# Kernel optimization log

Measured on AMD Instinct MI355X. Metric: run time of the kernel, lower is better.

Reference implementation:

```python
import jax, jax.numpy as jnp
import numpy as np

B, N, D_IN, D_OUT = 8, 2048, 256, 128
ROW_ZERO = 85 - 10  # hardcoded in original: a[:, 0:85-10] = 0 (zeros rows, dim 1)
NEG_BIG = -9.0e15
EPS = 1e-12  # F.normalize eps


def setup_inputs() -> dict:
    key = jax.random.key(0)
    k1, k2, k3, k4 = jax.random.split(key, 4)
    h = jax.random.normal(k1, (B, N, D_IN), dtype=jnp.float32)
    adj = jax.random.randint(k2, (B, N, N), 0, 2, dtype=jnp.int32)
    adj_eye = jax.random.randint(k3, (B, N, N), 0, 2, dtype=jnp.int32)
    # xavier_uniform with gain=1.414 for W [in, out]
    limit = 1.414 * np.sqrt(6.0 / (D_IN + D_OUT))
    W = jax.random.uniform(k4, (D_IN, D_OUT), minval=-limit, maxval=limit, dtype=jnp.float32)
    return {"h": h, "adj": adj, "adj_eye": adj_eye, "W": W}


def reference(h, adj, adj_eye, W):
    # Wh: [B, N, D_OUT]
    Wh = jnp.matmul(h, W)
    # L2-normalize along feature dim (F.normalize semantics: x / max(||x||, eps))
    norm = jnp.maximum(jnp.linalg.norm(Wh, axis=-1, keepdims=True), EPS)
    Whn = Wh / norm
    # dense cosine-similarity scores: [B, N, N]
    score = jnp.einsum("bnd,bmd->bnm", Whn, Whn)
    # double-sort top-k emulation (faithful to original, incl. row-wise zeroing bug)
    a_sorted = jnp.sort(score, axis=-1)
    idx1 = jnp.argsort(score, axis=-1)
    a_sorted = a_sorted.at[:, 0:ROW_ZERO, :].set(0.0)
    idx2 = jnp.argsort(idx1, axis=-1)  # inverse permutation
    attscore = jnp.take_along_axis(a_sorted, idx2, axis=-1)
    # adjacency mask + softmax over neighbors
    e = jnp.where(adj_eye > 0, attscore, NEG_BIG)
    attention = jax.nn.softmax(e, axis=-1)
    # (dropout is identity in eval mode)
    h_prime = jnp.matmul(attention, Wh)
    return jax.nn.elu(h_prime)
```

## Files before the change

### kernel.cpp

```cpp
#include <hip/hip_runtime.h>
#include <stdint.h>

#define NN   2048
#define DD   128
#define DIN  256
#define ROWZ 75

typedef float f32x4 __attribute__((ext_vector_type(4)));
typedef short bf16x8 __attribute__((ext_vector_type(8)));
typedef unsigned int u32x2 __attribute__((ext_vector_type(2)));

__device__ __forceinline__ unsigned short f2bf(float x){
  union { float f; unsigned int u; } v; v.f = x;
  unsigned int u = v.u;
  u += 0x7fffu + ((u >> 16) & 1u);
  return (unsigned short)(u >> 16);
}
__device__ __forceinline__ float bf2f(unsigned short b){
  union { float f; unsigned int u; } v; v.u = ((unsigned int)b) << 16;
  return v.f;
}

__launch_bounds__(512, 2)
__global__ void wh_kernel(const float* __restrict__ h, const float* __restrict__ W,
                          unsigned short* __restrict__ whn, unsigned short* __restrict__ whT)
{
  __shared__ unsigned short WhiT[128][40];
  __shared__ unsigned short WloT[128][40];
  __shared__ float ssp[64][3];
  __shared__ float sinv_s[64];

  const int t    = threadIdx.x;
  const int bid  = blockIdx.x;
  const int r0   = ((bid & 7) << 11) | ((bid >> 3) << 6);
  const int w    = t >> 6;
  const int l    = t & 63;
  const int quad = l >> 4;
  const int l16  = l & 15;
  const int wr   = (w & 3) * 16;
  const int nc   = (w >> 2) * 64;
  const int ch   = w >> 2;

  const int sd = t & 127;
  const int sk = (t >> 7) * 8;

  f32x4 acc[4], occ[4];
#pragma unroll
  for (int ns = 0; ns < 4; ++ns){
    acc[ns] = (f32x4){0.f,0.f,0.f,0.f};
    occ[ns] = (f32x4){0.f,0.f,0.f,0.f};
  }

  float wv[8];
#pragma unroll
  for (int j = 0; j < 8; ++j) wv[j] = W[(size_t)(sk + j) * DD + sd];
  const float* hrow = h + (size_t)(r0 + wr + l16) * DIN;
  f32x4 hv0 = *(const f32x4*)(hrow + quad*8);
  f32x4 hv1 = *(const f32x4*)(hrow + quad*8 + 4);

  for (int kt = 0; kt < 8; ++kt){
    __syncthreads();
    {
      bf16x8 whi8, wlo8;
#pragma unroll
      for (int j = 0; j < 8; ++j){
        float x = wv[j];
        unsigned short hb = f2bf(x);
        whi8[j] = (short)hb;
        wlo8[j] = (short)f2bf(x - bf2f(hb));
      }
      *(bf16x8*)&WhiT[sd][sk] = whi8;
      *(bf16x8*)&WloT[sd][sk] = wlo8;
    }
    bf16x8 ahi, alo;
#pragma unroll
    for (int e = 0; e < 4; ++e){
      unsigned short hb0 = f2bf(hv0[e]), hb1 = f2bf(hv1[e]);
      ahi[e]   = (short)hb0;  alo[e]   = (short)f2bf(hv0[e] - bf2f(hb0));
      ahi[4+e] = (short)hb1;  alo[4+e] = (short)f2bf(hv1[e] - bf2f(hb1));
    }
    __syncthreads();

    if (kt < 7){
      const int k0n = (kt + 1) * 32;
#pragma unroll
      for (int j = 0; j < 8; ++j) wv[j] = W[(size_t)(k0n + sk + j) * DD + sd];
      hv0 = *(const f32x4*)(hrow + k0n + quad*8);
      hv1 = *(const f32x4*)(hrow + k0n + quad*8 + 4);
    }

#pragma unroll
    for (int ns = 0; ns < 4; ++ns){
      bf16x8 bhi = *(const bf16x8*)&WhiT[nc + ns*16 + l16][quad*8];
      bf16x8 blo = *(const bf16x8*)&WloT[nc + ns*16 + l16][quad*8];
      acc[ns] = __builtin_amdgcn_mfma_f32_16x16x32_bf16(ahi, bhi, acc[ns], 0, 0, 0);
      acc[ns] = __builtin_amdgcn_mfma_f32_16x16x32_bf16(alo, bhi, acc[ns], 0, 0, 0);
      acc[ns] = __builtin_amdgcn_mfma_f32_16x16x32_bf16(ahi, blo, acc[ns], 0, 0, 0);
      occ[ns] = __builtin_amdgcn_mfma_f32_16x16x32_bf16(bhi, ahi, occ[ns], 0, 0, 0);
      occ[ns] = __builtin_amdgcn_mfma_f32_16x16x32_bf16(bhi, alo, occ[ns], 0, 0, 0);
      occ[ns] = __builtin_amdgcn_mfma_f32_16x16x32_bf16(blo, ahi, occ[ns], 0, 0, 0);
    }
  }

#pragma unroll
  for (int r = 0; r < 4; ++r){
    float val = 0.f;
#pragma unroll
    for (int ns = 0; ns < 4; ++ns) val += acc[ns][r] * acc[ns][r];
    val += __shfl_xor(val, 1);
    val += __shfl_xor(val, 2);
    val += __shfl_xor(val, 4);
    val += __shfl_xor(val, 8);
    if (l16 == 0) ssp[wr + quad*4 + r][ch] = val;
  }
  __syncthreads();
  if (t < 64){
    float ss = ssp[t][0] + ssp[t][1];
    sinv_s[t] = 1.0f / fmaxf(sqrtf(ss), 1e-12f);
  }
  __syncthreads();

  const int bb = r0 >> 11;
  const int n0 = (r0 & 2047) + wr;

#pragma unroll
  for (int ns = 0; ns < 4; ++ns)
#pragma unroll
    for (int r = 0; r < 4; ++r){
      const int row = wr + quad*4 + r;
      whn[(size_t)(r0 + row) * DD + nc + ns*16 + l16] = f2bf(acc[ns][r] * sinv_s[row]);
    }
#pragma unroll
  for (int ns = 0; ns < 4; ++ns)
#pragma unroll
    for (int r = 0; r < 4; ++r){
      const int d = nc + ns*16 + quad*4 + r;
      whT[((size_t)(bb * DD + d)) * NN + n0 + l16] = f2bf(occ[ns][r]);
    }
}

__launch_bounds__(512, 2)
__global__ void attn_kernel(const unsigned short* __restrict__ whn,
                            const unsigned short* __restrict__ whT,
                            const int* __restrict__ adje,
                            float* __restrict__ out)
{
  __shared__ unsigned short Kt[2][128 * 128];
  __shared__ unsigned short Vt[2][128 * 128];
  __shared__ unsigned short Pbuf[8][32 * 40];
  __shared__ float linv_s[64];

  const int t    = threadIdx.x;
  const int w    = t >> 6;
  const int l    = t & 63;
  const int quad = l >> 4;
  const int l16  = l & 15;
  const int qh   = w >> 2;
  const int ms   = w & 3;
  const int b     = blockIdx.x & 7;
  const int qbase = (blockIdx.x >> 3) * 64;

  const unsigned short* whn_b = whn + (size_t)b * NN * DD;
  const unsigned short* whT_b = whT + (size_t)b * DD * NN;
  const int*            adj_b = adje + (size_t)b * NN * NN;

#define STAGE(M0, CC)                                                          \
  if (w < 4){                                                                  \
    _Pragma("unroll")                                                          \
    for (int ii = 0; ii < 8; ++ii){                                            \
      const int row = w*32 + ii*4 + (l >> 4);                                  \
      const unsigned short* src = whn_b + (size_t)((M0) + row) * DD            \
                                  + (l16 ^ (row & 7)) * 8;                     \
      __builtin_amdgcn_global_load_lds(                                        \
          (const __attribute__((address_space(1))) void*)src,                  \
          (__attribute__((address_space(3))) void*)&Kt[CC][(w*32 + ii*4)*128], \
          16, 0, 0);                                                           \
    }                                                                          \
  } else {                                                                     \
    _Pragma("unroll")                                                          \
    for (int ii = 0; ii < 8; ++ii){                                            \
      const int dv = (w-4)*32 + ii*4 + (l >> 4);                               \
      const unsigned short* src = whT_b + (size_t)dv * NN + (M0)               \
                                  + (l16 ^ (dv & 7)) * 8;                      \
      __builtin_amdgcn_global_load_lds(                                        \
          (const __attribute__((address_space(1))) void*)src,                  \
          (__attribute__((address_space(3))) void*)&Vt[CC][((w-4)*32+ii*4)*128],\
          16, 0, 0);                                                           \
    }                                                                          \
  }

  bf16x8 qf[2][4];
#pragma unroll
  for (int s = 0; s < 2; ++s)
#pragma unroll
    for (int kc = 0; kc < 4; ++kc)
      qf[s][kc] = *(const bf16x8*)(whn_b + (size_t)(qbase + qh*32 + s*16 + l16) * DD + kc*32 + quad*8);

  f32x4 oacc[2][8];
  float lacc[2][4];
#pragma unroll
  for (int s = 0; s < 2; ++s){
#pragma unroll
    for (int dt = 0; dt < 8; ++dt) oacc[s][dt] = (f32x4){0.f, 0.f, 0.f, 0.f};
#pragma unroll
    for (int r = 0; r < 4; ++r) lacc[s][r] = 0.f;
  }

  unsigned short* const Pw = &Pbuf[w][0];

  int av[2][2][4];
#pragma unroll
  for (int f = 0; f < 2; ++f)
#pragma unroll
    for (int s = 0; s < 2; ++s)
#pragma unroll
      for (int r = 0; r < 4; ++r)
        av[f][s][r] = adj_b[(size_t)(qbase + qh*32 + s*16 + quad*4 + r) * NN + ms*32 + f*16 + l16];
  STAGE(0, 0)
  __syncthreads();

  for (int it = 0; it < 16; ++it){
    const int m0  = it * 128;
    const int cur = it & 1;

    int avn[2][2][4];
    if (it < 15){
      const int mn = m0 + 128;
#pragma unroll
      for (int f = 0; f < 2; ++f)
#pragma unroll
        for (int s = 0; s < 2; ++s)
#pragma unroll
          for (int r = 0; r < 4; ++r)
            avn[f][s][r] = adj_b[(size_t)(qbase + qh*32 + s*16 + quad*4 + r) * NN + mn + ms*32 + f*16 + l16];
      STAGE(mn, cur ^ 1)
    }

    bf16x8 kf[2][4];
#pragma unroll
    for (int f = 0; f < 2; ++f)
#pragma unroll
      for (int kc = 0; kc < 4; ++kc){
        const int row = ms*32 + f*16 + l16;
        kf[f][kc] = *(const bf16x8*)&Kt[cur][row*128 + (((kc*4 + quad) ^ (l16 & 7)) * 8)];
      }
#pragma unroll
    for (int f = 0; f < 2; ++f){
#pragma unroll
      for (int s = 0; s < 2; ++s){
        f32x4 sc = (f32x4){0.f, 0.f, 0.f, 0.f};
#pragma unroll
        for (int kc = 0; kc < 4; ++kc)
          sc = __builtin_amdgcn_mfma_f32_16x16x32_bf16(qf[s][kc], kf[f][kc], sc, 0, 0, 0);
#pragma unroll
        for (int r = 0; r < 4; ++r){
          const int qrow = qbase + qh*32 + s*16 + quad*4 + r;
          float sv = (qrow < ROWZ) ? 0.f : sc[r];
          float p32 = (av[f][s][r] > 0) ? __expf(sv) : 0.f;
          unsigned short pb = f2bf(p32);
          lacc[s][r] += bf2f(pb);
          Pw[(s*16 + quad*4 + r) * 40 + f*16 + l16] = pb;
        }
      }
    }

    bf16x8 pfr0 = *(const bf16x8*)&Pw[(l16) * 40 + quad*8];
    bf16x8 pfr1 = *(const bf16x8*)&Pw[(16 + l16) * 40 + quad*8];
    __builtin_amdgcn_s_setprio(1);
#pragma unroll
    for (int dt = 0; dt < 8; ++dt){
      const int d = dt*16 + l16;
      bf16x8 vf = *(const bf16x8*)&Vt[cur][d*128 + (((ms*4 + quad) ^ (l16 & 7)) * 8)];
      oacc[0][dt] = __builtin_amdgcn_mfma_f32_16x16x32_bf16(pfr0, vf, oacc[0][dt], 0, 0, 0);
      oacc[1][dt] = __builtin_amdgcn_mfma_f32_16x16x32_bf16(pfr1, vf, oacc[1][dt], 0, 0, 0);
    }
    __builtin_amdgcn_s_setprio(0);

    __builtin_amdgcn_sched_barrier(0);
    asm volatile("s_waitcnt vmcnt(0)" ::: "memory");
    __builtin_amdgcn_sched_barrier(0);
    __builtin_amdgcn_s_barrier();
    __builtin_amdgcn_sched_barrier(0);

    if (it < 15){
#pragma unroll
      for (int f = 0; f < 2; ++f)
#pragma unroll
        for (int s = 0; s < 2; ++s)
#pragma unroll
          for (int r = 0; r < 4; ++r)
            av[f][s][r] = avn[f][s][r];
    }
  }

  {
    float* fl = (float*)&Pbuf[0][0];
#pragma unroll
    for (int s = 0; s < 2; ++s)
#pragma unroll
      for (int r = 0; r < 4; ++r)
        fl[(qh*32 + s*16 + quad*4 + r) * 64 + ms*16 + l16] = lacc[s][r];
  }
  __syncthreads();
  if (t < 64){
    const float* fl = (const float*)&Pbuf[0][0];
    float sum = 0.f;
#pragma unroll
    for (int c = 0; c < 64; ++c) sum += fl[t * 64 + c];
    linv_s[t] = 1.0f / sum;
  }

  float* const owf = (float*)&Kt[0][0];
  for (int s = 0; s < 2; ++s){
    __syncthreads();
#pragma unroll
    for (int dt = 0; dt < 8; ++dt)
#pragma unroll
      for (int r = 0; r < 4; ++r)
        owf[w*2048 + (quad*4 + r)*128 + dt*16 + l16] = oacc[s][dt][r];
    __syncthreads();
#pragma unroll
    for (int j = 0; j < 8; ++j){
      const int o     = j*512 + t;
      const int row32 = o >> 7;
      const int d     = o & 127;
      const int qh2   = row32 >> 4;
      const int r16   = row32 & 15;
      float v = owf[(qh2*4 + 0)*2048 + r16*128 + d]
              + owf[(qh2*4 + 1)*2048 + r16*128 + d]
              + owf[(qh2*4 + 2)*2048 + r16*128 + d]
              + owf[(qh2*4 + 3)*2048 + r16*128 + d];
      const int qrl = qh2*32 + s*16 + r16;
      v *= linv_s[qrl];
      v = (v > 0.f) ? v : expm1f(v);
      out[(size_t)(b*NN + qbase + qrl) * DD + d] = v;
    }
  }
#undef STAGE
}

extern "C" void kernel_launch(void* const* d_in, const int* in_sizes, int n_in,
                              void* d_out, int out_size, void* d_ws, size_t ws_size,
                              hipStream_t stream)
{
  const float* h       = (const float*)d_in[0];
  const int*   adj_eye = (const int*)d_in[2];
  const float* W       = (const float*)d_in[3];
  float*       out     = (float*)d_out;

  unsigned short* whn  = (unsigned short*)d_ws;
  unsigned short* whT  = whn + (size_t)16384 * 128;

  wh_kernel<<<256, 512, 0, stream>>>(h, W, whn, whT);
  attn_kernel<<<256, 512, 0, stream>>>(whn, whT, adj_eye, out);
}
```

Before: 282.7 us.

## Pack adjacency mask into bitmasks in the Wh kernel before attention

Adds 256 extra blocks to the first kernel that read the int32 adjacency matrix and compress it into 64-bit ballot bitmasks in workspace. The attention kernel then reads 32-bit mask words per row instead of int32 values per element, which cuts the bytes it loads from global memory. The full int32 adjacency matrix still has to be read once by the packing blocks, adding a write and read of the small packed mask and extra work in the first launch. The attention mask loads are now issued in the same iteration they are used rather than prefetched one step ahead, which may expose their latency.

```diff
diff --git a/kernel.cpp b/kernel.cpp
--- a/kernel.cpp
+++ b/kernel.cpp
@@ -22,16 +22,45 @@
 }
 
 __launch_bounds__(512, 2)
-__global__ void wh_kernel(const float* __restrict__ h, const float* __restrict__ W,
-                          unsigned short* __restrict__ whn, unsigned short* __restrict__ whT)
+__global__ void wh_pack_kernel(const float* __restrict__ h, const float* __restrict__ W,
+                               const int* __restrict__ adje,
+                               unsigned short* __restrict__ whn, unsigned short* __restrict__ whT,
+                               unsigned long long* __restrict__ adjp)
 {
+  const int t   = threadIdx.x;
+  const int bid = blockIdx.x;
+
+  if (bid >= 256){
+    const int pb = bid - 256;
+    const int wv = t >> 6;
+    const int ln = t & 63;
+#pragma unroll 1
+    for (int rr = 0; rr < 8; ++rr){
+      const int grow = pb * 64 + wv * 8 + rr;
+      const int* arow = adje + (size_t)grow * NN;
+      unsigned long long* drow = adjp + (size_t)grow * 32;
+#pragma unroll 1
+      for (int cb = 0; cb < 2; ++cb){
+        int pv[16];
+#pragma unroll
+        for (int j = 0; j < 16; ++j) pv[j] = arow[(cb*16 + j) * 64 + ln];
+        unsigned long long m[16];
+#pragma unroll
+        for (int j = 0; j < 16; ++j) m[j] = __ballot(pv[j] > 0);
+        if (ln == 0){
+#pragma unroll
+          for (int j = 0; j < 16; ++j) drow[cb*16 + j] = m[j];
+        }
+      }
+    }
+    return;
+  }
+
   __shared__ unsigned short WhiT[128][40];
   __shared__ unsigned short WloT[128][40];
   __shared__ float ssp[64][3];
   __shared__ float sinv_s[64];
 
-  const int t    = threadIdx.x;
-  const int bid  = blockIdx.x;
   const int r0   = ((bid & 7) << 11) | ((bid >> 3) << 6);
   const int w    = t >> 6;
   const int l    = t & 63;
@@ -51,9 +80,9 @@
     occ[ns] = (f32x4){0.f,0.f,0.f,0.f};
   }
 
-  float wv[8];
-#pragma unroll
-  for (int j = 0; j < 8; ++j) wv[j] = W[(size_t)(sk + j) * DD + sd];
+  float wv8[8];
+#pragma unroll
+  for (int j = 0; j < 8; ++j) wv8[j] = W[(size_t)(sk + j) * DD + sd];
   const float* hrow = h + (size_t)(r0 + wr + l16) * DIN;
   f32x4 hv0 = *(const f32x4*)(hrow + quad*8);
   f32x4 hv1 = *(const f32x4*)(hrow + quad*8 + 4);
@@ -64,7 +93,7 @@
       bf16x8 whi8, wlo8;
 #pragma unroll
       for (int j = 0; j < 8; ++j){
-        float x = wv[j];
+        float x = wv8[j];
         unsigned short hb = f2bf(x);
         whi8[j] = (short)hb;
         wlo8[j] = (short)f2bf(x - bf2f(hb));
@@ -84,7 +113,7 @@
     if (kt < 7){
       const int k0n = (kt + 1) * 32;
 #pragma unroll
-      for (int j = 0; j < 8; ++j) wv[j] = W[(size_t)(k0n + sk + j) * DD + sd];
+      for (int j = 0; j < 8; ++j) wv8[j] = W[(size_t)(k0n + sk + j) * DD + sd];
       hv0 = *(const f32x4*)(hrow + k0n + quad*8);
       hv1 = *(const f32x4*)(hrow + k0n + quad*8 + 4);
     }
@@ -142,7 +171,7 @@
 __launch_bounds__(512, 2)
 __global__ void attn_kernel(const unsigned short* __restrict__ whn,
                             const unsigned short* __restrict__ whT,
-                            const int* __restrict__ adje,
+                            const unsigned int* __restrict__ adjp,
                             float* __restrict__ out)
 {
   __shared__ unsigned short Kt[2][128 * 128];
@@ -162,7 +191,7 @@
 
   const unsigned short* whn_b = whn + (size_t)b * NN * DD;
   const unsigned short* whT_b = whT + (size_t)b * DD * NN;
-  const int*            adj_b = adje + (size_t)b * NN * NN;
+  const unsigned int*   mrow  = adjp + ((size_t)(b * NN + qbase + qh*32)) * 64;
 
 #define STAGE(M0, CC)                                                          \
   if (w < 4){                                                                  \
@@ -208,14 +237,6 @@
 
   unsigned short* const Pw = &Pbuf[w][0];
 
-  int av[2][2][4];
-#pragma unroll
-  for (int f = 0; f < 2; ++f)
-#pragma unroll
-    for (int s = 0; s < 2; ++s)
-#pragma unroll
-      for (int r = 0; r < 4; ++r)
-        av[f][s][r] = adj_b[(size_t)(qbase + qh*32 + s*16 + quad*4 + r) * NN + ms*32 + f*16 + l16];
   STAGE(0, 0)
   __syncthreads();
 
@@ -223,18 +244,17 @@
     const int m0  = it * 128;
     const int cur = it & 1;
 
-    int avn[2][2][4];
     if (it < 15){
       const int mn = m0 + 128;
-#pragma unroll
-      for (int f = 0; f < 2; ++f)
-#pragma unroll
-        for (int s = 0; s < 2; ++s)
-#pragma unroll
-          for (int r = 0; r < 4; ++r)
-            avn[f][s][r] = adj_b[(size_t)(qbase + qh*32 + s*16 + quad*4 + r) * NN + mn + ms*32 + f*16 + l16];
       STAGE(mn, cur ^ 1)
     }
+
+    unsigned int mw[2][4];
+#pragma unroll
+    for (int s = 0; s < 2; ++s)
+#pragma unroll
+      for (int r = 0; r < 4; ++r)
+        mw[s][r] = mrow[(size_t)(s*16 + quad*4 + r) * 64 + it*4 + ms];
 
     bf16x8 kf[2][4];
 #pragma unroll
@@ -256,7 +276,7 @@
         for (int r = 0; r < 4; ++r){
           const int qrow = qbase + qh*32 + s*16 + quad*4 + r;
           float sv = (qrow < ROWZ) ? 0.f : sc[r];
-          float p32 = (av[f][s][r] > 0) ? __expf(sv) : 0.f;
+          float p32 = ((mw[s][r] >> (f*16 + l16)) & 1u) ? __expf(sv) : 0.f;
           unsigned short pb = f2bf(p32);
           lacc[s][r] += bf2f(pb);
           Pw[(s*16 + quad*4 + r) * 40 + f*16 + l16] = pb;
@@ -281,16 +301,6 @@
     __builtin_amdgcn_sched_barrier(0);
     __builtin_amdgcn_s_barrier();
     __builtin_amdgcn_sched_barrier(0);
-
-    if (it < 15){
-#pragma unroll
-      for (int f = 0; f < 2; ++f)
-#pragma unroll
-        for (int s = 0; s < 2; ++s)
-#pragma unroll
-          for (int r = 0; r < 4; ++r)
-            av[f][s][r] = avn[f][s][r];
-    }
   }
 
   {
@@ -350,7 +360,8 @@
 
   unsigned short* whn  = (unsigned short*)d_ws;
   unsigned short* whT  = whn + (size_t)16384 * 128;
-
-  wh_kernel<<<256, 512, 0, stream>>>(h, W, whn, whT);
-  attn_kernel<<<256, 512, 0, stream>>>(whn, whT, adj_eye, out);
-}
+  unsigned long long* adjp = (unsigned long long*)(whT + (size_t)16384 * 128);
+
+  wh_pack_kernel<<<512, 512, 0, stream>>>(h, W, adj_eye, whn, whT, adjp);
+  attn_kernel<<<256, 512, 0, stream>>>(whn, whT, (const unsigned int*)adjp, out);
+}
```

Result: slower. 299.7 us (+6.0%).

## Double-buffer adjacency loads with partial vmcnt wait and split Wh rows across more blocks

Applied to the files above, without the earlier changes.

The attention loop now issues the next tile's stage before the adjacency loads, keeps adjacency in a parity-indexed double buffer, fully unrolls the loop, and waits only until at most 16 vector-memory ops are outstanding, so the next tile's adjacency loads can stay in flight across the barrier. This removes the register copy of the prefetched adjacency and the full vmcnt(0) drain each iteration. Separately, the Wh kernel processes 32 rows per block, with each wave covering 32 columns, and launches 512 blocks for more parallelism. The risks are a more fragile vmcnt count tied to the instruction order, and extra register pressure from the unrolled loop and duplicated adjacency buffers.

```diff
diff --git a/kernel.cpp b/kernel.cpp
--- a/kernel.cpp
+++ b/kernel.cpp
@@ -27,34 +27,33 @@
 {
   __shared__ unsigned short WhiT[128][40];
   __shared__ unsigned short WloT[128][40];
-  __shared__ float ssp[64][3];
-  __shared__ float sinv_s[64];
+  __shared__ float ssp[32][5];
+  __shared__ float sinv_s[32];
 
   const int t    = threadIdx.x;
   const int bid  = blockIdx.x;
-  const int r0   = ((bid & 7) << 11) | ((bid >> 3) << 6);
+  const int r0   = ((bid & 7) << 11) | ((bid >> 3) << 5);
   const int w    = t >> 6;
   const int l    = t & 63;
   const int quad = l >> 4;
   const int l16  = l & 15;
-  const int wr   = (w & 3) * 16;
-  const int nc   = (w >> 2) * 64;
-  const int ch   = w >> 2;
+  const int rg   = w >> 2;
+  const int cs   = w & 3;
 
   const int sd = t & 127;
   const int sk = (t >> 7) * 8;
 
-  f32x4 acc[4], occ[4];
-#pragma unroll
-  for (int ns = 0; ns < 4; ++ns){
+  f32x4 acc[2], occ[2];
+#pragma unroll
+  for (int ns = 0; ns < 2; ++ns){
     acc[ns] = (f32x4){0.f,0.f,0.f,0.f};
     occ[ns] = (f32x4){0.f,0.f,0.f,0.f};
   }
 
-  float wv[8];
-#pragma unroll
-  for (int j = 0; j < 8; ++j) wv[j] = W[(size_t)(sk + j) * DD + sd];
-  const float* hrow = h + (size_t)(r0 + wr + l16) * DIN;
+  float wv8[8];
+#pragma unroll
+  for (int j = 0; j < 8; ++j) wv8[j] = W[(size_t)(sk + j) * DD + sd];
+  const float* hrow = h + (size_t)(r0 + rg*16 + l16) * DIN;
   f32x4 hv0 = *(const f32x4*)(hrow + quad*8);
   f32x4 hv1 = *(const f32x4*)(hrow + quad*8 + 4);
 
@@ -64,7 +63,7 @@
       bf16x8 whi8, wlo8;
 #pragma unroll
       for (int j = 0; j < 8; ++j){
-        float x = wv[j];
+        float x = wv8[j];
         unsigned short hb = f2bf(x);
         whi8[j] = (short)hb;
         wlo8[j] = (short)f2bf(x - bf2f(hb));
@@ -84,15 +83,15 @@
     if (kt < 7){
       const int k0n = (kt + 1) * 32;
 #pragma unroll
-      for (int j = 0; j < 8; ++j) wv[j] = W[(size_t)(k0n + sk + j) * DD + sd];
+      for (int j = 0; j < 8; ++j) wv8[j] = W[(size_t)(k0n + sk + j) * DD + sd];
       hv0 = *(const f32x4*)(hrow + k0n + quad*8);
       hv1 = *(const f32x4*)(hrow + k0n + quad*8 + 4);
     }
 
 #pragma unroll
-    for (int ns = 0; ns < 4; ++ns){
-      bf16x8 bhi = *(const bf16x8*)&WhiT[nc + ns*16 + l16][quad*8];
-      bf16x8 blo = *(const bf16x8*)&WloT[nc + ns*16 + l16][quad*8];
+    for (int ns = 0; ns < 2; ++ns){
+      bf16x8 bhi = *(const bf16x8*)&WhiT[cs*32 + ns*16 + l16][quad*8];
+      bf16x8 blo = *(const bf16x8*)&WloT[cs*32 + ns*16 + l16][quad*8];
       acc[ns] = __builtin_amdgcn_mfma_f32_16x16x32_bf16(ahi, bhi, acc[ns], 0, 0, 0);
       acc[ns] = __builtin_amdgcn_mfma_f32_16x16x32_bf16(alo, bhi, acc[ns], 0, 0, 0);
       acc[ns] = __builtin_amdgcn_mfma_f32_16x16x32_bf16(ahi, blo, acc[ns], 0, 0, 0);
@@ -104,37 +103,35 @@
 
 #pragma unroll
   for (int r = 0; r < 4; ++r){
-    float val = 0.f;
-#pragma unroll
-    for (int ns = 0; ns < 4; ++ns) val += acc[ns][r] * acc[ns][r];
+    float val = acc[0][r]*acc[0][r] + acc[1][r]*acc[1][r];
     val += __shfl_xor(val, 1);
     val += __shfl_xor(val, 2);
     val += __shfl_xor(val, 4);
     val += __shfl_xor(val, 8);
-    if (l16 == 0) ssp[wr + quad*4 + r][ch] = val;
+    if (l16 == 0) ssp[rg*16 + quad*4 + r][cs] = val;
   }
   __syncthreads();
-  if (t < 64){
-    float ss = ssp[t][0] + ssp[t][1];
+  if (t < 32){
+    float ss = ssp[t][0] + ssp[t][1] + ssp[t][2] + ssp[t][3];
     sinv_s[t] = 1.0f / fmaxf(sqrtf(ss), 1e-12f);
   }
   __syncthreads();
 
   const int bb = r0 >> 11;
-  const int n0 = (r0 & 2047) + wr;
-
-#pragma unroll
-  for (int ns = 0; ns < 4; ++ns)
+  const int n0 = (r0 & 2047) + rg*16;
+
+#pragma unroll
+  for (int ns = 0; ns < 2; ++ns)
 #pragma unroll
     for (int r = 0; r < 4; ++r){
-      const int row = wr + quad*4 + r;
-      whn[(size_t)(r0 + row) * DD + nc + ns*16 + l16] = f2bf(acc[ns][r] * sinv_s[row]);
-    }
-#pragma unroll
-  for (int ns = 0; ns < 4; ++ns)
+      const int row = rg*16 + quad*4 + r;
+      whn[(size_t)(r0 + row) * DD + cs*32 + ns*16 + l16] = f2bf(acc[ns][r] * sinv_s[row]);
+    }
+#pragma unroll
+  for (int ns = 0; ns < 2; ++ns)
 #pragma unroll
     for (int r = 0; r < 4; ++r){
-      const int d = nc + ns*16 + quad*4 + r;
+      const int d = cs*32 + ns*16 + quad*4 + r;
       whT[((size_t)(bb * DD + d)) * NN + n0 + l16] = f2bf(occ[ns][r]);
     }
 }
@@ -208,32 +205,33 @@
 
   unsigned short* const Pw = &Pbuf[w][0];
 
-  int av[2][2][4];
+  int av[2][2][2][4];
 #pragma unroll
   for (int f = 0; f < 2; ++f)
 #pragma unroll
     for (int s = 0; s < 2; ++s)
 #pragma unroll
       for (int r = 0; r < 4; ++r)
-        av[f][s][r] = adj_b[(size_t)(qbase + qh*32 + s*16 + quad*4 + r) * NN + ms*32 + f*16 + l16];
+        av[0][f][s][r] = adj_b[(size_t)(qbase + qh*32 + s*16 + quad*4 + r) * NN + ms*32 + f*16 + l16];
   STAGE(0, 0)
   __syncthreads();
 
+#pragma unroll
   for (int it = 0; it < 16; ++it){
     const int m0  = it * 128;
     const int cur = it & 1;
-
-    int avn[2][2][4];
+    const int par = it & 1;
+
     if (it < 15){
       const int mn = m0 + 128;
+      STAGE(mn, cur ^ 1)
 #pragma unroll
       for (int f = 0; f < 2; ++f)
 #pragma unroll
         for (int s = 0; s < 2; ++s)
 #pragma unroll
           for (int r = 0; r < 4; ++r)
-            avn[f][s][r] = adj_b[(size_t)(qbase + qh*32 + s*16 + quad*4 + r) * NN + mn + ms*32 + f*16 + l16];
-      STAGE(mn, cur ^ 1)
+            av[par ^ 1][f][s][r] = adj_b[(size_t)(qbase + qh*32 + s*16 + quad*4 + r) * NN + mn + ms*32 + f*16 + l16];
     }
 
     bf16x8 kf[2][4];
@@ -256,7 +254,7 @@
         for (int r = 0; r < 4; ++r){
           const int qrow = qbase + qh*32 + s*16 + quad*4 + r;
           float sv = (qrow < ROWZ) ? 0.f : sc[r];
-          float p32 = (av[f][s][r] > 0) ? __expf(sv) : 0.f;
+          float p32 = (av[par][f][s][r] > 0) ? __expf(sv) : 0.f;
           unsigned short pb = f2bf(p32);
           lacc[s][r] += bf2f(pb);
           Pw[(s*16 + quad*4 + r) * 40 + f*16 + l16] = pb;
@@ -277,20 +275,10 @@
     __builtin_amdgcn_s_setprio(0);
 
     __builtin_amdgcn_sched_barrier(0);
-    asm volatile("s_waitcnt vmcnt(0)" ::: "memory");
+    asm volatile("s_waitcnt vmcnt(16)" ::: "memory");
     __builtin_amdgcn_sched_barrier(0);
     __builtin_amdgcn_s_barrier();
     __builtin_amdgcn_sched_barrier(0);
-
-    if (it < 15){
-#pragma unroll
-      for (int f = 0; f < 2; ++f)
-#pragma unroll
-        for (int s = 0; s < 2; ++s)
-#pragma unroll
-          for (int r = 0; r < 4; ++r)
-            av[f][s][r] = avn[f][s][r];
-    }
   }
 
   {
@@ -351,6 +339,6 @@
   unsigned short* whn  = (unsigned short*)d_ws;
   unsigned short* whT  = whn + (size_t)16384 * 128;
 
-  wh_kernel<<<256, 512, 0, stream>>>(h, W, whn, whT);
+  wh_kernel<<<512, 512, 0, stream>>>(h, W, whn, whT);
   attn_kernel<<<256, 512, 0, stream>>>(whn, whT, adj_eye, out);
 }
```

New measurement: 360.3 us. +27.4%, slower.
